# Kernel optimization log

Hardware: AMD Instinct MI355X
Metric: run time of the kernel (lower is better)

The kernel has to match this reference:

```python
import math
import jax, jax.numpy as jnp
import numpy as np

B, T, C, H = 2, 2048, 1024, 16
HD = C // H

def gelu_tanh(x):
    # 0.5*x*(1+tanh(sqrt(2/pi)*(x+0.044715*x^3)))
    c = math.sqrt(2.0 / math.pi)
    return 0.5 * x * (1.0 + jnp.tanh(c * (x + 0.044715 * x * x * x)))

def layernorm(x, g, b, eps=1e-5):
    mu = jnp.mean(x, axis=-1, keepdims=True)
    var = jnp.var(x, axis=-1, keepdims=True)
    return (x - mu) * jax.lax.rsqrt(var + eps) * g + b

def setup_inputs() -> dict:
    key = jax.random.key(0)
    ks = jax.random.split(key, 6)
    s = 0.02
    return {
        "x": jax.random.normal(ks[0], (B, T, C), jnp.float32),
        "ln1_g": jnp.ones((C,), jnp.float32),
        "ln1_b": jnp.zeros((C,), jnp.float32),
        "W_qkv": jax.random.normal(ks[1], (C, 3 * C), jnp.float32) * s,
        "b_qkv": jnp.zeros((3 * C,), jnp.float32),
        "W_out": jax.random.normal(ks[2], (C, C), jnp.float32) * s,
        "b_out": jnp.zeros((C,), jnp.float32),
        "ln2_g": jnp.ones((C,), jnp.float32),
        "ln2_b": jnp.zeros((C,), jnp.float32),
        "W_fc1": jax.random.normal(ks[3], (C, 4 * C), jnp.float32) * s,
        "b_fc1": jnp.zeros((4 * C,), jnp.float32),
        "W_fc2": jax.random.normal(ks[4], (4 * C, C), jnp.float32) * s,
        "b_fc2": jnp.zeros((C,), jnp.float32),
    }

def reference(x, ln1_g, ln1_b, W_qkv, b_qkv, W_out, b_out,
              ln2_g, ln2_b, W_fc1, b_fc1, W_fc2, b_fc2):
    # pre-LN causal self-attention
    h = layernorm(x, ln1_g, ln1_b)
    qkv = h @ W_qkv + b_qkv                      # [B,T,3C]
    q, k, v = jnp.split(qkv, 3, axis=-1)
    q = q.reshape(B, T, H, HD).transpose(0, 2, 1, 3)  # [B,H,T,HD]
    k = k.reshape(B, T, H, HD).transpose(0, 2, 1, 3)
    v = v.reshape(B, T, H, HD).transpose(0, 2, 1, 3)
    scores = jnp.einsum("bhqd,bhkd->bhqk", q, k) * (1.0 / math.sqrt(HD))
    causal = jnp.tril(jnp.ones((T, T), bool))
    scores = jnp.where(causal, scores, jnp.float32(-jnp.inf))
    att = jax.nn.softmax(scores, axis=-1)
    out = jnp.einsum("bhqk,bhkd->bhqd", att, v)  # [B,H,T,HD]
    out = out.transpose(0, 2, 1, 3).reshape(B, T, C)
    out = out @ W_out + b_out
    temp = x + out
    # GELU MLP
    h2 = layernorm(temp, ln2_g, ln2_b)
    ff = gelu_tanh(h2 @ W_fc1 + b_fc1) @ W_fc2 + b_fc2
    return temp + ff
```

## Files before the change

### kernel.cpp

```cpp
#include <hip/hip_runtime.h>
#include <stdint.h>

#define Bb 2
#define Tt 2048
#define Cc 1024
#define Hh 16
#define HD 64
#define Mm (Bb*Tt)

typedef __bf16 bf16x8 __attribute__((ext_vector_type(8)));
typedef float  f32x4  __attribute__((ext_vector_type(4)));

#define DEV static __device__ __forceinline__

DEV float asfloat_(uint32_t u){ union{uint32_t u; float f;} x; x.u=u; return x.f; }
DEV uint32_t asuint_(float f){ union{float f; uint32_t u;} x; x.f=f; return x.u; }
DEV unsigned short f2bf(float f){
  uint32_t u = asuint_(f);
  uint32_t r = (u + 0x7fffu + ((u>>16)&1u)) >> 16;
  return (unsigned short)r;
}
DEV float gelu_(float x){
  float x3 = x*x*x;
  float t  = 0.7978845608028654f * (x + 0.044715f*x3);
  float e  = __expf(2.0f*t);
  float th = 1.0f - 2.0f/(e + 1.0f);
  return 0.5f * x * (1.0f + th);
}

#define GLL(gsrc, ldst) __builtin_amdgcn_global_load_lds( \
    (const __attribute__((address_space(1))) void*)(gsrc), \
    (__attribute__((address_space(3))) void*)(ldst), 16, 0, 0)

__global__ void wcvt_kernel(const float* __restrict__ W, unsigned short* __restrict__ WT,
                            int K, int N) {
  __shared__ float tile[32][33];
  int tx = threadIdx.x & 31, ty = threadIdx.x >> 5;
  int kb = blockIdx.x * 32, nb = blockIdx.y * 32;
  #pragma unroll
  for (int r = 0; r < 32; r += 8)
    tile[ty + r][tx] = W[(size_t)(kb + ty + r) * N + nb + tx];
  __syncthreads();
  #pragma unroll
  for (int r = 0; r < 32; r += 8)
    WT[(size_t)(nb + ty + r) * K + kb + tx] = f2bf(tile[tx][ty + r]);
}

__global__ void ln_kernel(const float* __restrict__ X, const float* __restrict__ g,
                          const float* __restrict__ bb, unsigned short* __restrict__ O) {
  int row = blockIdx.x, t = threadIdx.x;
  const float4* xr = (const float4*)(X + (size_t)row * Cc);
  float4 v = xr[t];
  float s = v.x + v.y + v.z + v.w;
  float q = v.x*v.x + v.y*v.y + v.z*v.z + v.w*v.w;
  #pragma unroll
  for (int o = 32; o > 0; o >>= 1) { s += __shfl_xor(s, o); q += __shfl_xor(q, o); }
  __shared__ float ss[4], sq[4];
  int w = t >> 6;
  if ((t & 63) == 0) { ss[w] = s; sq[w] = q; }
  __syncthreads();
  s = ss[0] + ss[1] + ss[2] + ss[3];
  q = sq[0] + sq[1] + sq[2] + sq[3];
  float mu  = s * (1.0f/Cc);
  float var = q * (1.0f/Cc) - mu*mu;
  float rstd = rsqrtf(var + 1e-5f);
  float4 gv = ((const float4*)g)[t], bv = ((const float4*)bb)[t];
  ushort4 o4;
  o4.x = f2bf((v.x-mu)*rstd*gv.x + bv.x);
  o4.y = f2bf((v.y-mu)*rstd*gv.y + bv.y);
  o4.z = f2bf((v.z-mu)*rstd*gv.z + bv.z);
  o4.w = f2bf((v.w-mu)*rstd*gv.w + bv.w);
  ((ushort4*)(O + (size_t)row * Cc))[t] = o4;
}

template<int MODE>
__launch_bounds__(512, 4)
__global__ void gemm_kernel(const unsigned short* __restrict__ A,
                            const unsigned short* __restrict__ BT,
                            const float* __restrict__ bias,
                            const float* __restrict__ res,
                            void* __restrict__ Cout,
                            int N, int K) {
  __shared__ unsigned short As[128*64];
  __shared__ unsigned short Bs[128*64];
  int tid  = threadIdx.x;
  int lane = tid & 63, w = tid >> 6;
  int wr = w >> 2, wc = w & 3;
  int g = lane >> 4, ql = lane & 15;
  int bm = blockIdx.x, bn = blockIdx.y;

  f32x4 acc[4][2];
  #pragma unroll
  for (int m = 0; m < 4; ++m)
    #pragma unroll
    for (int n = 0; n < 2; ++n) acc[m][n] = (f32x4){0.f,0.f,0.f,0.f};

  int r  = tid >> 3;
  int cc = tid & 7;
  int sc = (cc ^ (r & 7)) * 8;
  const unsigned short* Ag = A  + (size_t)(bm*128 + r) * K + sc;
  const unsigned short* Bg = BT + (size_t)(bn*128 + r) * K + sc;
  int sw = (ql & 7) << 3;
  int nk = K >> 6;

  for (int kt = 0; kt < nk; ++kt) {
    if (kt) __syncthreads();
    const unsigned short* ag = Ag + kt*64;
    const unsigned short* bg = Bg + kt*64;
    GLL(ag,                  As + w*512);
    GLL(ag + (size_t)64*K,   As + 4096 + w*512);
    GLL(bg,                  Bs + w*512);
    GLL(bg + (size_t)64*K,   Bs + 4096 + w*512);
    __syncthreads();

    #pragma unroll
    for (int kk = 0; kk < 2; ++kk) {
      int col = (kk*32 + g*8) ^ sw;
      bf16x8 af[4], bf2[2];
      #pragma unroll
      for (int m = 0; m < 4; ++m)
        af[m] = *(const bf16x8*)(As + (wr*64 + m*16 + ql)*64 + col);
      #pragma unroll
      for (int n = 0; n < 2; ++n)
        bf2[n] = *(const bf16x8*)(Bs + (wc*32 + n*16 + ql)*64 + col);
      #pragma unroll
      for (int m = 0; m < 4; ++m)
        #pragma unroll
        for (int n = 0; n < 2; ++n)
          acc[m][n] = __builtin_amdgcn_mfma_f32_16x16x32_bf16(af[m], bf2[n], acc[m][n], 0, 0, 0);
    }
  }

  int r0 = bm*128 + wr*64;
  int c0 = bn*128 + wc*32;
  int lr = g * 4;
  #pragma unroll
  for (int m = 0; m < 4; ++m) {
    #pragma unroll
    for (int n = 0; n < 2; ++n) {
      int col = c0 + n*16 + ql;
      float bv = bias[col];
      #pragma unroll
      for (int i = 0; i < 4; ++i) {
        int row = r0 + m*16 + lr + i;
        float v = acc[m][n][i] + bv;
        if (MODE == 1 || MODE == 3) v += res[(size_t)row * N + col];
        if (MODE == 2) v = gelu_(v);
        if (MODE == 0 || MODE == 2)
          ((unsigned short*)Cout)[(size_t)row * N + col] = f2bf(v);
        else
          ((float*)Cout)[(size_t)row * N + col] = v;
      }
    }
  }
}

__global__ void vtr_kernel(const unsigned short* __restrict__ qkv,
                           unsigned short* __restrict__ vtb) {
  __shared__ unsigned short Tl[64][72];
  int tid = threadIdx.x;
  int bh = blockIdx.x, tc = blockIdx.y;
  int b = bh >> 4, h = bh & 15;
  int r = tid >> 2, c0 = (tid & 3) * 16;
  const unsigned short* src = qkv + (size_t)(b*Tt + tc*64 + r)*3072 + 2048 + h*64 + c0;
  *(int4*)&Tl[r][c0]     = *(const int4*)(src);
  *(int4*)&Tl[r][c0 + 8] = *(const int4*)(src + 8);
  __syncthreads();
  int d = tid >> 2, k0 = (tid & 3) * 16;
  ushort4 o[4];
  #pragma unroll
  for (int jj = 0; jj < 4; ++jj) {
    o[jj].x = Tl[k0 + jj*4 + 0][d];
    o[jj].y = Tl[k0 + jj*4 + 1][d];
    o[jj].z = Tl[k0 + jj*4 + 2][d];
    o[jj].w = Tl[k0 + jj*4 + 3][d];
  }
  unsigned short* dst = vtb + ((size_t)(bh*64 + d))*2048 + tc*64 + k0;
  *(int4*)(dst)     = *(int4*)&o[0];
  *(int4*)(dst + 8) = *(int4*)&o[2];
}

__global__ __launch_bounds__(512, 4)
void attn_kernel(const unsigned short* __restrict__ qkv,
                 const unsigned short* __restrict__ vtb,
                 unsigned short* __restrict__ att) {
  __shared__ __align__(16) char smem[36864];
  int tid  = threadIdx.x;
  int lane = tid & 63, w = tid >> 6;
  int g = lane >> 4, ql = lane & 15;

  int bid = blockIdx.x;
  int bh = bid & 31;
  int jj = bid >> 5;
  int j  = (jj < 8) ? (2*jj) : (31 - 2*jj);
  int b = bh >> 4, h = bh & 15;
  int Q0 = j * 128;
  int qbase = Q0 + w * 16;
  char* Pb = smem + 16384 + w * 2560;

  const unsigned short* qrow = qkv + (size_t)(b*Tt + qbase + ql) * 3072 + h*64;
  bf16x8 qf0 = *(const bf16x8*)(qrow + g*8);
  bf16x8 qf1 = *(const bf16x8*)(qrow + 32 + g*8);

  f32x4 O[4];
  #pragma unroll
  for (int d = 0; d < 4; ++d) O[d] = (f32x4){0.f,0.f,0.f,0.f};
  float mrun = -1e30f, lrun = 0.f;

  int nt = Q0/64 + 2;

  int srow = tid >> 3;
  int scol = (tid & 7) * 8;
  int wr_off = srow*128 + ((scol*2) ^ ((srow & 7) << 4));
  const unsigned short* Kg = qkv + (size_t)(b*Tt + srow)*3072 + 1024 + h*64 + scol;
  const unsigned short* Vg = vtb + ((size_t)(bh*64 + srow))*2048 + scol;

  int4 kreg = *(const int4*)(Kg);
  int4 vreg = *(const int4*)(Vg);

  for (int t0 = 0; t0 < nt; ++t0) {
    __syncthreads();
    *(int4*)(smem + wr_off)        = kreg;
    *(int4*)(smem + 8192 + wr_off) = vreg;
    __syncthreads();
    if (t0 + 1 < nt) {
      kreg = *(const int4*)(Kg + (size_t)(t0+1)*64*3072);
      vreg = *(const int4*)(Vg + (t0+1)*64);
    }
    if (t0*64 > qbase + 15) continue;

    bool full = (t0*64 + 63) <= qbase;
    float ps[16];
    #pragma unroll
    for (int s = 0; s < 4; ++s) {
      int krow = s*16 + ql;
      int kb0 = krow*128 + (( g*16      ) ^ ((krow&7)<<4));
      int kb1 = krow*128 + (( g*16 + 64 ) ^ ((krow&7)<<4));
      bf16x8 kf0 = *(const bf16x8*)(smem + kb0);
      bf16x8 kf1 = *(const bf16x8*)(smem + kb1);
      f32x4 a = (f32x4){0.f,0.f,0.f,0.f};
      a = __builtin_amdgcn_mfma_f32_16x16x32_bf16(kf0, qf0, a, 0, 0, 0);
      a = __builtin_amdgcn_mfma_f32_16x16x32_bf16(kf1, qf1, a, 0, 0, 0);
      #pragma unroll
      for (int i = 0; i < 4; ++i) ps[s*4+i] = a[i] * 0.125f;
    }
    if (!full) {
      #pragma unroll
      for (int s = 0; s < 4; ++s)
        #pragma unroll
        for (int i = 0; i < 4; ++i)
          if (t0*64 + s*16 + g*4 + i > qbase + ql) ps[s*4+i] = -1e30f;
    }
    float tm = ps[0];
    #pragma unroll
    for (int i = 1; i < 16; ++i) tm = fmaxf(tm, ps[i]);
    tm = fmaxf(tm, __shfl_xor(tm, 16));
    tm = fmaxf(tm, __shfl_xor(tm, 32));
    float mnew = fmaxf(mrun, tm);
    float corr = __expf(mrun - mnew);
    float tsum = 0.f;
    #pragma unroll
    for (int s = 0; s < 4; ++s) {
      float e0 = __expf(ps[s*4+0] - mnew);
      float e1 = __expf(ps[s*4+1] - mnew);
      float e2 = __expf(ps[s*4+2] - mnew);
      float e3 = __expf(ps[s*4+3] - mnew);
      tsum += (e0 + e1) + (e2 + e3);
      ushort4 pk;
      pk.x = f2bf(e0); pk.y = f2bf(e1); pk.z = f2bf(e2); pk.w = f2bf(e3);
      *(ushort4*)(Pb + ql*160 + s*32 + g*8) = pk;
    }
    tsum += __shfl_xor(tsum, 16);
    tsum += __shfl_xor(tsum, 32);
    lrun = lrun * corr + tsum;
    mrun = mnew;

    float c0 = __shfl(corr, g*4 + 0);
    float c1 = __shfl(corr, g*4 + 1);
    float c2 = __shfl(corr, g*4 + 2);
    float c3 = __shfl(corr, g*4 + 3);
    #pragma unroll
    for (int d = 0; d < 4; ++d) {
      O[d][0] *= c0; O[d][1] *= c1; O[d][2] *= c2; O[d][3] *= c3;
    }
    #pragma unroll
    for (int kk = 0; kk < 2; ++kk) {
      bf16x8 pf = *(const bf16x8*)(Pb + ql*160 + kk*64 + g*16);
      #pragma unroll
      for (int d = 0; d < 4; ++d) {
        int drow = d*16 + ql;
        int vb = drow*128 + ((kk*64 + g*16) ^ ((drow&7)<<4));
        bf16x8 vf = *(const bf16x8*)(smem + 8192 + vb);
        O[d] = __builtin_amdgcn_mfma_f32_16x16x32_bf16(pf, vf, O[d], 0, 0, 0);
      }
    }
  }

  float l0 = __shfl(lrun, g*4 + 0);
  float l1 = __shfl(lrun, g*4 + 1);
  float l2 = __shfl(lrun, g*4 + 2);
  float l3 = __shfl(lrun, g*4 + 3);
  #pragma unroll
  for (int d = 0; d < 4; ++d) {
    size_t base = (size_t)(b*Tt + qbase)*Cc + h*64 + d*16 + ql;
    att[base + (size_t)(g*4+0)*Cc] = f2bf(O[d][0] / l0);
    att[base + (size_t)(g*4+1)*Cc] = f2bf(O[d][1] / l1);
    att[base + (size_t)(g*4+2)*Cc] = f2bf(O[d][2] / l2);
    att[base + (size_t)(g*4+3)*Cc] = f2bf(O[d][3] / l3);
  }
}

extern "C" void kernel_launch(void* const* d_in, const int* in_sizes, int n_in,
                              void* d_out, int out_size, void* d_ws, size_t ws_size,
                              hipStream_t stream) {
  const float* x    = (const float*)d_in[0];
  const float* ln1g = (const float*)d_in[1];
  const float* ln1b = (const float*)d_in[2];
  const float* Wqkv = (const float*)d_in[3];
  const float* bqkv = (const float*)d_in[4];
  const float* Wout = (const float*)d_in[5];
  const float* bout = (const float*)d_in[6];
  const float* ln2g = (const float*)d_in[7];
  const float* ln2b = (const float*)d_in[8];
  const float* Wfc1 = (const float*)d_in[9];
  const float* bfc1 = (const float*)d_in[10];
  const float* Wfc2 = (const float*)d_in[11];
  const float* bfc2 = (const float*)d_in[12];

  char* ws = (char*)d_ws;
  unsigned short* wqkvT = (unsigned short*)(ws);
  unsigned short* woutT = (unsigned short*)(ws + (6u<<20));
  unsigned short* wfc1T = (unsigned short*)(ws + (8u<<20));
  unsigned short* wfc2T = (unsigned short*)(ws + (16u<<20));
  unsigned short* vtb   = (unsigned short*)(ws + (24u<<20));
  float*          temp  = (float*)(ws + (24u<<20));
  unsigned short* hbuf  = (unsigned short*)(ws + (40u<<20));
  unsigned short* qkvb  = (unsigned short*)(ws + (48u<<20));
  unsigned short* attb  = (unsigned short*)(ws + (72u<<20));
  unsigned short* a1b   = (unsigned short*)(ws + (48u<<20));

  dim3 b256(256), b512(512);
  wcvt_kernel<<<dim3(1024/32, 3072/32), b256, 0, stream>>>(Wqkv, wqkvT, 1024, 3072);
  wcvt_kernel<<<dim3(1024/32, 1024/32), b256, 0, stream>>>(Wout, woutT, 1024, 1024);
  wcvt_kernel<<<dim3(1024/32, 4096/32), b256, 0, stream>>>(Wfc1, wfc1T, 1024, 4096);
  wcvt_kernel<<<dim3(4096/32, 1024/32), b256, 0, stream>>>(Wfc2, wfc2T, 4096, 1024);

  ln_kernel<<<Mm, b256, 0, stream>>>(x, ln1g, ln1b, hbuf);
  gemm_kernel<0><<<dim3(Mm/128, 3072/128), b512, 0, stream>>>(hbuf, wqkvT, bqkv, nullptr, qkvb, 3072, 1024);
  vtr_kernel<<<dim3(32, 32), b256, 0, stream>>>(qkvb, vtb);
  attn_kernel<<<dim3(512), 512, 0, stream>>>(qkvb, vtb, attb);
  gemm_kernel<1><<<dim3(Mm/128, 1024/128), b512, 0, stream>>>(attb, woutT, bout, x, temp, 1024, 1024);
  ln_kernel<<<Mm, b256, 0, stream>>>(temp, ln2g, ln2b, hbuf);
  gemm_kernel<2><<<dim3(Mm/128, 4096/128), b512, 0, stream>>>(hbuf, wfc1T, bfc1, nullptr, a1b, 4096, 1024);
  gemm_kernel<3><<<dim3(Mm/128, 1024/128), b512, 0, stream>>>(a1b, wfc2T, bfc2, temp, d_out, 1024, 4096);
}
```

Baseline: 368.4 us.

## Add intra-block split-K GEMM for the two narrow N=1024 projections

Adds a 1024-thread GEMM kernel that splits K into two halves. Each half is handled by one 512-thread group with its own LDS buffers, and the partial accumulators are reduced through shared memory before the bias and residual epilogue. It replaces the out-projection and fc2 GEMMs, whose 256-block grids underfill the GPU, to double the waves per tile and improve latency hiding. The cost is extra LDS traffic and barriers for the reduction, higher LDS use per block, and half the threads sitting idle in the epilogue.

```diff
diff --git a/kernel.cpp b/kernel.cpp
--- a/kernel.cpp
+++ b/kernel.cpp
@@ -144,12 +144,112 @@
       for (int i = 0; i < 4; ++i) {
         int row = r0 + m*16 + lr + i;
         float v = acc[m][n][i] + bv;
-        if (MODE == 1 || MODE == 3) v += res[(size_t)row * N + col];
         if (MODE == 2) v = gelu_(v);
-        if (MODE == 0 || MODE == 2)
-          ((unsigned short*)Cout)[(size_t)row * N + col] = f2bf(v);
-        else
-          ((float*)Cout)[(size_t)row * N + col] = v;
+        ((unsigned short*)Cout)[(size_t)row * N + col] = f2bf(v);
+      }
+    }
+  }
+}
+
+__launch_bounds__(1024, 2)
+__global__ void gemm_skrf_kernel(const unsigned short* __restrict__ A,
+                                 const unsigned short* __restrict__ BT,
+                                 const float* __restrict__ bias,
+                                 const float* __restrict__ res,
+                                 float* __restrict__ Cout,
+                                 int N, int K) {
+  __shared__ __align__(16) unsigned short SMEM[32768];
+  int tid  = threadIdx.x;
+  int lane = tid & 63, w = tid >> 6;
+  int wg = w >> 3, w8 = w & 7;
+  int wr = w8 >> 2, wc = w8 & 3;
+  int g = lane >> 4, ql = lane & 15;
+  int bm = blockIdx.x, bn = blockIdx.y;
+
+  unsigned short* AsH = SMEM + wg*8192;
+  unsigned short* BsH = SMEM + 16384 + wg*8192;
+
+  f32x4 acc[4][2];
+  #pragma unroll
+  for (int m = 0; m < 4; ++m)
+    #pragma unroll
+    for (int n = 0; n < 2; ++n) acc[m][n] = (f32x4){0.f,0.f,0.f,0.f};
+
+  int tid_h = tid & 511;
+  int r  = tid_h >> 3;
+  int cc = tid_h & 7;
+  int sc = (cc ^ (r & 7)) * 8;
+  int kbase = wg * (K >> 1);
+  const unsigned short* Ag = A  + (size_t)(bm*128 + r) * K + kbase + sc;
+  const unsigned short* Bg = BT + (size_t)(bn*128 + r) * K + kbase + sc;
+  int sw = (ql & 7) << 3;
+  int nk = K >> 7;
+
+  for (int kt = 0; kt < nk; ++kt) {
+    if (kt) __syncthreads();
+    const unsigned short* ag = Ag + kt*64;
+    const unsigned short* bg = Bg + kt*64;
+    GLL(ag,                  AsH + w8*512);
+    GLL(ag + (size_t)64*K,   AsH + 4096 + w8*512);
+    GLL(bg,                  BsH + w8*512);
+    GLL(bg + (size_t)64*K,   BsH + 4096 + w8*512);
+    __syncthreads();
+
+    #pragma unroll
+    for (int kk = 0; kk < 2; ++kk) {
+      int col = (kk*32 + g*8) ^ sw;
+      bf16x8 af[4], bf2[2];
+      #pragma unroll
+      for (int m = 0; m < 4; ++m)
+        af[m] = *(const bf16x8*)(AsH + (wr*64 + m*16 + ql)*64 + col);
+      #pragma unroll
+      for (int n = 0; n < 2; ++n)
+        bf2[n] = *(const bf16x8*)(BsH + (wc*32 + n*16 + ql)*64 + col);
+      #pragma unroll
+      for (int m = 0; m < 4; ++m)
+        #pragma unroll
+        for (int n = 0; n < 2; ++n)
+          acc[m][n] = __builtin_amdgcn_mfma_f32_16x16x32_bf16(af[m], bf2[n], acc[m][n], 0, 0, 0);
+    }
+  }
+
+  __syncthreads();
+  float* ex = (float*)SMEM;
+  int eb = (w8*64 + lane) * 32;
+  if (wg == 1) {
+    #pragma unroll
+    for (int m = 0; m < 4; ++m)
+      #pragma unroll
+      for (int n = 0; n < 2; ++n) {
+        int c = m*2 + n;
+        *(f32x4*)&ex[eb + ((c ^ (lane & 7)) << 2)] = acc[m][n];
+      }
+  }
+  __syncthreads();
+  if (wg == 0) {
+    #pragma unroll
+    for (int m = 0; m < 4; ++m)
+      #pragma unroll
+      for (int n = 0; n < 2; ++n) {
+        int c = m*2 + n;
+        f32x4 o = *(const f32x4*)&ex[eb + ((c ^ (lane & 7)) << 2)];
+        acc[m][n][0] += o[0]; acc[m][n][1] += o[1];
+        acc[m][n][2] += o[2]; acc[m][n][3] += o[3];
+      }
+    int r0 = bm*128 + wr*64;
+    int c0 = bn*128 + wc*32;
+    int lr = g * 4;
+    #pragma unroll
+    for (int m = 0; m < 4; ++m) {
+      #pragma unroll
+      for (int n = 0; n < 2; ++n) {
+        int col = c0 + n*16 + ql;
+        float bv = bias[col];
+        #pragma unroll
+        for (int i = 0; i < 4; ++i) {
+          int row = r0 + m*16 + lr + i;
+          Cout[(size_t)row * N + col] = acc[m][n][i] + bv + res[(size_t)row * N + col];
+        }
       }
     }
   }
@@ -339,7 +439,7 @@
   unsigned short* attb  = (unsigned short*)(ws + (72u<<20));
   unsigned short* a1b   = (unsigned short*)(ws + (48u<<20));
 
-  dim3 b256(256), b512(512);
+  dim3 b256(256), b512(512), b1024(1024);
   wcvt_kernel<<<dim3(1024/32, 3072/32), b256, 0, stream>>>(Wqkv, wqkvT, 1024, 3072);
   wcvt_kernel<<<dim3(1024/32, 1024/32), b256, 0, stream>>>(Wout, woutT, 1024, 1024);
   wcvt_kernel<<<dim3(1024/32, 4096/32), b256, 0, stream>>>(Wfc1, wfc1T, 1024, 4096);
@@ -349,8 +449,8 @@
   gemm_kernel<0><<<dim3(Mm/128, 3072/128), b512, 0, stream>>>(hbuf, wqkvT, bqkv, nullptr, qkvb, 3072, 1024);
   vtr_kernel<<<dim3(32, 32), b256, 0, stream>>>(qkvb, vtb);
   attn_kernel<<<dim3(512), 512, 0, stream>>>(qkvb, vtb, attb);
-  gemm_kernel<1><<<dim3(Mm/128, 1024/128), b512, 0, stream>>>(attb, woutT, bout, x, temp, 1024, 1024);
+  gemm_skrf_kernel<<<dim3(Mm/128, 1024/128), b1024, 0, stream>>>(attb, woutT, bout, x, temp, 1024, 1024);
   ln_kernel<<<Mm, b256, 0, stream>>>(temp, ln2g, ln2b, hbuf);
   gemm_kernel<2><<<dim3(Mm/128, 4096/128), b512, 0, stream>>>(hbuf, wfc1T, bfc1, nullptr, a1b, 4096, 1024);
-  gemm_kernel<3><<<dim3(Mm/128, 1024/128), b512, 0, stream>>>(a1b, wfc2T, bfc2, temp, d_out, 1024, 4096);
-}
+  gemm_skrf_kernel<<<dim3(Mm/128, 1024/128), b1024, 0, stream>>>(a1b, wfc2T, bfc2, temp, (float*)d_out, 1024, 4096);
+}
```

Measured after the change: 356.1 us. 1.03x faster.
